# Performance work log

Measured on AMD Instinct MI355X. Metric: run time of the kernel, lower is better.

Reference implementation:

```python
import jax, jax.numpy as jnp
import numpy as np

B, S, K, N = 2, 512, 4096, 16384

def setup_inputs() -> dict:
    key = jax.random.key(0)
    k1, k2, k3, k4 = jax.random.split(key, 4)
    x = jax.random.normal(k1, (B, S, K), dtype=jnp.float32)
    # int8-valued quantized weight stored as int32 (values in [-128, 127])
    weight_quant = jax.random.randint(k2, (N, K), -128, 128, dtype=jnp.int32)
    # per-output-row scale, positive and away from zero (quantize_weight clamps min=1e-8)
    scale = jax.random.uniform(k3, (N,), dtype=jnp.float32, minval=0.001, maxval=0.02)
    bias = jax.random.normal(k4, (N,), dtype=jnp.float32)
    return {"x": x, "weight_quant": weight_quant, "scale": scale, "bias": bias}

def reference(x, weight_quant, scale, bias):
    # Dequantize: weight[n,k] = float(weight_quant[n,k]) * scale[n]
    weight = weight_quant.astype(jnp.float32) * scale[:, None]  # [N, K]
    # F.linear: x @ weight.T + bias
    return jnp.einsum('bsk,nk->bsn', x, weight) + bias
```

## Files before the change

### kernel.cpp

```cpp
#include <hip/hip_runtime.h>

typedef __attribute__((ext_vector_type(4))) float f32x4;
typedef __attribute__((ext_vector_type(4))) int   i32x4;

static constexpr int Kd = 4096, Nd = 16384, Md = 1024;
static constexpr int BK = 128;
static constexpr int NT = Kd / BK;


__device__ __forceinline__ void gload16(const char* g, char* l) {
    __builtin_amdgcn_global_load_lds(
        (const __attribute__((address_space(1))) void*)g,
        (__attribute__((address_space(3))) void*)l, 16, 0, 0);
}

__device__ __forceinline__ int pack4(int a, int b, int c, int d) {
    return (a & 255) | ((b & 255) << 8) | ((c & 255) << 16) | (d << 24);
}


__global__ __launch_bounds__(256) void convert_w_kernel(
    const int* __restrict__ wq, char* __restrict__ wb) {
    const int ngroups = (Nd / 16) * Kd;
    int g = blockIdx.x * 256 + threadIdx.x;
    const int stride = gridDim.x * 256;
    for (; g < ngroups; g += stride) {
        const int* src = wq + (size_t)g * 16;
        i32x4 a = *(const i32x4*)(src);
        i32x4 b = *(const i32x4*)(src + 4);
        i32x4 c = *(const i32x4*)(src + 8);
        i32x4 d = *(const i32x4*)(src + 12);
        i32x4 o;
        o[0] = pack4(a[0], a[1], a[2], a[3]);
        o[1] = pack4(b[0], b[1], b[2], b[3]);
        o[2] = pack4(c[0], c[1], c[2], c[3]);
        o[3] = pack4(d[0], d[1], d[2], d[3]);
        *(i32x4*)(wb + (size_t)g * 16) = o;
    }
}


__global__ __launch_bounds__(256) void convert_x_kernel(
    const float* __restrict__ x, char* __restrict__ xb, float* __restrict__ xs) {
    const int row = blockIdx.x;
    const int t   = threadIdx.x;
    const float* xr = x + (size_t)row * Kd;

    f32x4 v[4];
    float amax = 0.f;
    #pragma unroll
    for (int i = 0; i < 4; ++i) {
        v[i] = *(const f32x4*)(xr + t * 16 + i * 4);
        #pragma unroll
        for (int j = 0; j < 4; ++j) amax = fmaxf(amax, fabsf(v[i][j]));
    }
    #pragma unroll
    for (int off = 32; off; off >>= 1)
        amax = fmaxf(amax, __shfl_xor(amax, off));
    __shared__ float wmax[4];
    if ((t & 63) == 0) wmax[t >> 6] = amax;
    __syncthreads();
    amax = fmaxf(fmaxf(wmax[0], wmax[1]), fmaxf(wmax[2], wmax[3]));
    amax = fmaxf(amax, 1e-20f);

    const float inv = 127.0f / amax;
    i32x4 o;
    #pragma unroll
    for (int i = 0; i < 4; ++i) {
        int q[4];
        #pragma unroll
        for (int j = 0; j < 4; ++j) {
            int qi = __float2int_rn(v[i][j] * inv);
            qi = qi > 127 ? 127 : (qi < -127 ? -127 : qi);
            q[j] = qi;
        }
        o[i] = pack4(q[0], q[1], q[2], q[3]);
    }
    *(i32x4*)(xb + (size_t)row * Kd + t * 16) = o;
    if (t == 0) xs[row] = amax * (1.0f / 127.0f);
}


#define BARRIER() asm volatile("s_barrier" ::: "memory")

#define LGKM0_FENCE() do {                                                     \
    asm volatile("s_waitcnt lgkmcnt(0)");                                      \
    __builtin_amdgcn_sched_barrier(0);                                         \
} while (0)

#define STAGE_A(slot, h, kt) do {                                              \
    char* lb_ = &LDS[slot][0][h][w * 8][0];                                    \
    gload16(Ab + (aRow0 + (h) * 64) * (size_t)Kd + (kt) * BK + gcol, lb_);     \
    gload16(Ab + (aRow0 + (h) * 64 + 128) * (size_t)Kd + (kt) * BK + gcol,     \
            lb_ + 64 * 128);                                                   \
} while (0)

#define STAGE_B(slot, j, kt) do {                                              \
    char* lb_ = &LDS[slot][1][j][w * 8][0];                                    \
    gload16(Bw + (bRow0 + (j) * 32) * (size_t)Kd + (kt) * BK + gcol, lb_);     \
    gload16(Bw + (bRow0 + (j) * 32 + 128) * (size_t)Kd + (kt) * BK + gcol,     \
            lb_ + 64 * 128);                                                   \
} while (0)

#define READ_A(dst, slot, h) do {                                              \
    const char* lA_ = &LDS[slot][0][h][0][0];                                  \
    _Pragma("unroll")                                                          \
    for (int mi = 0; mi < 4; ++mi)                                             \
        _Pragma("unroll")                                                      \
        for (int kk = 0; kk < 2; ++kk) {                                       \
            const int row_ = wm * 64 + mi * 16 + lr;                           \
            const int col_ = (l4 * 16 + kk * 64) ^ xorv;                       \
            dst[mi][kk] = *(const i32x4*)(lA_ + row_ * 128 + col_);            \
        }                                                                      \
} while (0)

#define READ_B(dst, slot, j) do {                                              \
    const char* lB_ = &LDS[slot][1][j][0][0];                                  \
    _Pragma("unroll")                                                          \
    for (int ni = 0; ni < 2; ++ni)                                             \
        _Pragma("unroll")                                                      \
        for (int kk = 0; kk < 2; ++kk) {                                       \
            const int row_ = wn * 32 + ni * 16 + lr;                           \
            const int col_ = (l4 * 16 + kk * 64) ^ xorv;                       \
            dst[ni][kk] = *(const i32x4*)(lB_ + row_ * 128 + col_);            \
        }                                                                      \
} while (0)

#define MFMA_QUAD(h, j, AF, BF) do {                                           \
    __builtin_amdgcn_s_setprio(1);                                             \
    _Pragma("unroll")                                                          \
    for (int mi = 0; mi < 4; ++mi)                                             \
        _Pragma("unroll")                                                      \
        for (int ni = 0; ni < 2; ++ni)                                         \
            _Pragma("unroll")                                                  \
            for (int kk = 0; kk < 2; ++kk)                                     \
                acc[(h) * 4 + mi][(j) * 2 + ni] =                              \
                    __builtin_amdgcn_mfma_i32_16x16x64_i8(                     \
                        AF[mi][kk], BF[ni][kk],                                \
                        acc[(h) * 4 + mi][(j) * 2 + ni], 0, 0, 0);             \
    __builtin_amdgcn_s_setprio(0);                                             \
} while (0)

#define VMCNT_TILE(t)                                                          \
    do {                                                                       \
        if ((t) + 2 < NT) asm volatile("s_waitcnt vmcnt(4)" ::: "memory");     \
        else              asm volatile("s_waitcnt vmcnt(0)" ::: "memory");     \
    } while (0)

#define TILE(slot, oslot, t) do {                                              \
    i32x4 afA[4][2], afB[4][2], bfA[2][2], bfB[2][2];                          \
                                                       \
    READ_A(afA, slot, 0);                                                      \
    READ_B(bfA, slot, 0);                                                      \
    if ((t) + 1 < NT) STAGE_A(oslot, 1, (t) + 1);                              \
    BARRIER(); LGKM0_FENCE();                                                  \
    MFMA_QUAD(0, 0, afA, bfA);                                                 \
    BARRIER();                                                                 \
                                                       \
    READ_B(bfB, slot, 1);                                                      \
    if ((t) + 1 < NT) STAGE_B(oslot, 1, (t) + 1);                              \
    BARRIER(); LGKM0_FENCE();                                                  \
    MFMA_QUAD(0, 1, afA, bfB);                                                 \
    BARRIER();                                                                 \
                                                       \
    READ_A(afB, slot, 1);                                                      \
    if ((t) + 2 < NT) STAGE_A(slot, 0, (t) + 2);                               \
    BARRIER(); LGKM0_FENCE();                                                  \
    MFMA_QUAD(1, 0, afB, bfA);                                                 \
    BARRIER();                                                                 \
                          \
    if ((t) + 2 < NT) STAGE_B(slot, 0, (t) + 2);                               \
    VMCNT_TILE(t);                                                             \
    BARRIER();                                                                 \
    MFMA_QUAD(1, 1, afB, bfB);                                                 \
    BARRIER();                                                                 \
} while (0)

__global__ __launch_bounds__(512, 2) void gemm8_kernel(
    const char* __restrict__ Ab,
    const char* __restrict__ Bw,
    const float* __restrict__ sw,
    const float* __restrict__ xs,
    const float* __restrict__ bias,
    float* __restrict__ C) {

    __shared__ __align__(16) char LDS[2][2][2][128][128];

    const int tid = threadIdx.x;
    const int l   = tid & 63;
    const int w   = tid >> 6;
    const int wm  = w >> 2;
    const int wn  = w & 3;
    const int lr  = l & 15;
    const int l4  = l >> 4;
    const int xorv = (lr & 7) << 4;

    const int orig = blockIdx.x;
    const int work = (orig & 7) * 32 + (orig >> 3);
    const int gm0 = (work & 3) * 256;
    const int gn0 = (work >> 2) * 256;

    const int g_log = (l & 7) ^ ((l >> 3) & 7);
    const int gcol  = g_log * 16;
    const size_t aRow0 = (size_t)(gm0 + w * 8 + (l >> 3));
    const size_t bRow0 = (size_t)(gn0 + (w >> 2) * 64 + (w & 3) * 8 + (l >> 3));

    i32x4 acc[8][4];
    #pragma unroll
    for (int i = 0; i < 8; ++i)
        #pragma unroll
        for (int j = 0; j < 4; ++j) {
            i32x4 z = {0, 0, 0, 0};
            acc[i][j] = z;
        }

    STAGE_A(0, 0, 0); STAGE_B(0, 0, 0);
    STAGE_A(0, 1, 0); STAGE_B(0, 1, 0);
    STAGE_A(1, 0, 1); STAGE_B(1, 0, 1);
    asm volatile("s_waitcnt vmcnt(4)" ::: "memory");
    BARRIER();

    #pragma unroll 1
    for (int tt = 0; tt < NT / 2; ++tt) {
        TILE(0, 1, 2 * tt);
        TILE(1, 0, 2 * tt + 1);
    }

    #pragma unroll
    for (int bj = 0; bj < 4; ++bj) {
        const int gn = gn0 + wn * 64 + bj * 16 + lr;
        const float sc = sw[gn];
        const float bi = bias[gn];
        #pragma unroll
        for (int ai = 0; ai < 8; ++ai) {
            const int gm = gm0 + wm * 128 + ai * 16 + l4 * 4;
            #pragma unroll
            for (int r = 0; r < 4; ++r)
                C[(size_t)(gm + r) * Nd + gn] =
                    (float)acc[ai][bj][r] * (sc * xs[gm + r]) + bi;
        }
    }
}


__global__ __launch_bounds__(256) void naive_kernel(
    const float* __restrict__ x, const int* __restrict__ wq,
    const float* __restrict__ scale, const float* __restrict__ bias,
    float* __restrict__ out) {
    const int n = blockIdx.x * 256 + threadIdx.x;
    const int m = blockIdx.y;
    if (n >= Nd) return;
    const float* xr = x + (size_t)m * Kd;
    const int*   wr = wq + (size_t)n * Kd;
    float s = 0.f;
    for (int k = 0; k < Kd; ++k) s += xr[k] * (float)wr[k];
    out[(size_t)m * Nd + n] = s * scale[n] + bias[n];
}


extern "C" void kernel_launch(void* const* d_in, const int* in_sizes, int n_in,
                              void* d_out, int out_size, void* d_ws, size_t ws_size,
                              hipStream_t stream) {
    const float* x     = (const float*)d_in[0];
    const int*   wq    = (const int*)d_in[1];
    const float* scale = (const float*)d_in[2];
    const float* bias  = (const float*)d_in[3];
    float* out = (float*)d_out;

    const size_t w_bytes = (size_t)Nd * Kd;
    const size_t x_bytes = (size_t)Md * Kd;
    const size_t s_bytes = (size_t)Md * sizeof(float);
    if (ws_size >= w_bytes + x_bytes + s_bytes && d_ws != nullptr) {
        char*  wb = (char*)d_ws;
        char*  xb = wb + w_bytes;
        float* xs = (float*)(xb + x_bytes);
        convert_w_kernel<<<4096, 256, 0, stream>>>(wq, wb);
        convert_x_kernel<<<Md, 256, 0, stream>>>(x, xb, xs);
        gemm8_kernel<<<256, 512, 0, stream>>>(xb, wb, scale, xs, bias, out);
    } else {
        dim3 grid(Nd / 256, Md);
        naive_kernel<<<grid, 256, 0, stream>>>(x, wq, scale, bias, out);
    }
}
```

Measured before the change: 142.9 us.

## Pre-swizzle int8 weights into MFMA fragment order and load B directly to registers

The weight conversion kernel now writes int8 weights in a per-wave, per-lane MFMA fragment layout, so the GEMM can load B fragments straight from global memory into registers with coalesced 16-byte loads. This drops the B tiles from LDS, halving LDS use, and removes the B LDS reads along with several barriers. The main loop is rewritten with explicit vmcnt waits and double-buffered B fragment registers. The cost is more register pressure, and B is no longer shared through LDS, so each wave row re-reads its B fragments from global or cache.

```diff
diff --git a/kernel.cpp b/kernel.cpp
--- a/kernel.cpp
+++ b/kernel.cpp
@@ -21,21 +21,30 @@
 
 __global__ __launch_bounds__(256) void convert_w_kernel(
     const int* __restrict__ wq, char* __restrict__ wb) {
-    const int ngroups = (Nd / 16) * Kd;
-    int g = blockIdx.x * 256 + threadIdx.x;
+    const int total = (Nd / 256) * NT * 4 * 8 * 64;
+    int c = blockIdx.x * 256 + threadIdx.x;
     const int stride = gridDim.x * 256;
-    for (; g < ngroups; g += stride) {
-        const int* src = wq + (size_t)g * 16;
+    for (; c < total; c += stride) {
+        const int l   = c & 63;
+        const int fid = (c >> 6) & 7;
+        const int wn  = (c >> 9) & 3;
+        const int kt  = (c >> 11) & 31;
+        const int nt  = c >> 16;
+        const int j   = fid >> 2, ni = (fid >> 1) & 1, kkb = fid & 1;
+        const int lr  = l & 15,   l4 = l >> 4;
+        const int n   = nt * 256 + wn * 64 + j * 32 + ni * 16 + lr;
+        const int k0  = kt * 128 + kkb * 64 + l4 * 16;
+        const int* src = wq + (size_t)n * Kd + k0;
         i32x4 a = *(const i32x4*)(src);
         i32x4 b = *(const i32x4*)(src + 4);
-        i32x4 c = *(const i32x4*)(src + 8);
+        i32x4 cc = *(const i32x4*)(src + 8);
         i32x4 d = *(const i32x4*)(src + 12);
         i32x4 o;
         o[0] = pack4(a[0], a[1], a[2], a[3]);
         o[1] = pack4(b[0], b[1], b[2], b[3]);
-        o[2] = pack4(c[0], c[1], c[2], c[3]);
+        o[2] = pack4(cc[0], cc[1], cc[2], cc[3]);
         o[3] = pack4(d[0], d[1], d[2], d[3]);
-        *(i32x4*)(wb + (size_t)g * 16) = o;
+        *((i32x4*)wb + c) = o;
     }
 }
 
@@ -82,28 +91,40 @@
 
 
 #define BARRIER() asm volatile("s_barrier" ::: "memory")
+#define SBAR() __builtin_amdgcn_sched_barrier(0)
 
 #define LGKM0_FENCE() do {                                                     \
     asm volatile("s_waitcnt lgkmcnt(0)");                                      \
     __builtin_amdgcn_sched_barrier(0);                                         \
 } while (0)
 
-#define STAGE_A(slot, h, kt) do {                                              \
-    char* lb_ = &LDS[slot][0][h][w * 8][0];                                    \
-    gload16(Ab + (aRow0 + (h) * 64) * (size_t)Kd + (kt) * BK + gcol, lb_);     \
-    gload16(Ab + (aRow0 + (h) * 64 + 128) * (size_t)Kd + (kt) * BK + gcol,     \
-            lb_ + 64 * 128);                                                   \
-} while (0)
-
-#define STAGE_B(slot, j, kt) do {                                              \
-    char* lb_ = &LDS[slot][1][j][w * 8][0];                                    \
-    gload16(Bw + (bRow0 + (j) * 32) * (size_t)Kd + (kt) * BK + gcol, lb_);     \
-    gload16(Bw + (bRow0 + (j) * 32 + 128) * (size_t)Kd + (kt) * BK + gcol,     \
-            lb_ + 64 * 128);                                                   \
+#define VMCNT(n) do {                                                          \
+    asm volatile("s_waitcnt vmcnt(" #n ")" ::: "memory");                      \
+    __builtin_amdgcn_sched_barrier(0);                                         \
+} while (0)
+
+#define STAGE_AFULL(slot, kt) do {                                             \
+    _Pragma("unroll")                                                          \
+    for (int h_ = 0; h_ < 2; ++h_) {                                           \
+        char* lb_ = &LDSA[slot][h_][w * 8][0];                                 \
+        gload16(Ab + (aRow0 + h_ * 64) * (size_t)Kd + (kt) * BK + gcol, lb_);  \
+        gload16(Ab + (aRow0 + h_ * 64 + 128) * (size_t)Kd + (kt) * BK + gcol,  \
+                lb_ + 64 * 128);                                               \
+    }                                                                          \
+    __builtin_amdgcn_sched_barrier(0);                                         \
+} while (0)
+
+#define LOAD_BF(buf, kt, jj) do {                                              \
+    const i32x4* p_ = Bfr + (size_t)(kt) * 2048 + wn * 512 + (jj) * 256 + l;   \
+    buf[0][0] = p_[0];                                                         \
+    buf[0][1] = p_[64];                                                        \
+    buf[1][0] = p_[128];                                                       \
+    buf[1][1] = p_[192];                                                       \
+    __builtin_amdgcn_sched_barrier(0);                                         \
 } while (0)
 
 #define READ_A(dst, slot, h) do {                                              \
-    const char* lA_ = &LDS[slot][0][h][0][0];                                  \
+    const char* lA_ = &LDSA[slot][h][0][0];                                    \
     _Pragma("unroll")                                                          \
     for (int mi = 0; mi < 4; ++mi)                                             \
         _Pragma("unroll")                                                      \
@@ -111,18 +132,6 @@
             const int row_ = wm * 64 + mi * 16 + lr;                           \
             const int col_ = (l4 * 16 + kk * 64) ^ xorv;                       \
             dst[mi][kk] = *(const i32x4*)(lA_ + row_ * 128 + col_);            \
-        }                                                                      \
-} while (0)
-
-#define READ_B(dst, slot, j) do {                                              \
-    const char* lB_ = &LDS[slot][1][j][0][0];                                  \
-    _Pragma("unroll")                                                          \
-    for (int ni = 0; ni < 2; ++ni)                                             \
-        _Pragma("unroll")                                                      \
-        for (int kk = 0; kk < 2; ++kk) {                                       \
-            const int row_ = wn * 32 + ni * 16 + lr;                           \
-            const int col_ = (l4 * 16 + kk * 64) ^ xorv;                       \
-            dst[ni][kk] = *(const i32x4*)(lB_ + row_ * 128 + col_);            \
         }                                                                      \
 } while (0)
 
@@ -141,38 +150,25 @@
     __builtin_amdgcn_s_setprio(0);                                             \
 } while (0)
 
-#define VMCNT_TILE(t)                                                          \
-    do {                                                                       \
-        if ((t) + 2 < NT) asm volatile("s_waitcnt vmcnt(4)" ::: "memory");     \
-        else              asm volatile("s_waitcnt vmcnt(0)" ::: "memory");     \
-    } while (0)
-
-#define TILE(slot, oslot, t) do {                                              \
-    i32x4 afA[4][2], afB[4][2], bfA[2][2], bfB[2][2];                          \
-                                                       \
-    READ_A(afA, slot, 0);                                                      \
-    READ_B(bfA, slot, 0);                                                      \
-    if ((t) + 1 < NT) STAGE_A(oslot, 1, (t) + 1);                              \
-    BARRIER(); LGKM0_FENCE();                                                  \
-    MFMA_QUAD(0, 0, afA, bfA);                                                 \
-    BARRIER();                                                                 \
-                                                       \
-    READ_B(bfB, slot, 1);                                                      \
-    if ((t) + 1 < NT) STAGE_B(oslot, 1, (t) + 1);                              \
-    BARRIER(); LGKM0_FENCE();                                                  \
-    MFMA_QUAD(0, 1, afA, bfB);                                                 \
-    BARRIER();                                                                 \
-                                                       \
-    READ_A(afB, slot, 1);                                                      \
-    if ((t) + 2 < NT) STAGE_A(slot, 0, (t) + 2);                               \
-    BARRIER(); LGKM0_FENCE();                                                  \
-    MFMA_QUAD(1, 0, afB, bfA);                                                 \
-    BARRIER();                                                                 \
-                          \
-    if ((t) + 2 < NT) STAGE_B(slot, 0, (t) + 2);                               \
-    VMCNT_TILE(t);                                                             \
-    BARRIER();                                                                 \
-    MFMA_QUAD(1, 1, afB, bfB);                                                 \
+#define TILE(slot, oslot, BF0USE, BF0NXT, t) do {                              \
+    if ((t) + 1 < NT) {                                                        \
+        STAGE_AFULL(oslot, (t) + 1);                                           \
+        LOAD_BF(BF0NXT, (t) + 1, 0);                                           \
+    }                                                                          \
+    READ_A(af, slot, 0);                                                       \
+    if ((t) + 1 < NT) { VMCNT(12); } else { VMCNT(4); }                        \
+    LGKM0_FENCE();                                                             \
+    MFMA_QUAD(0, 0, af, BF0USE);                                               \
+    if ((t) + 1 < NT) { VMCNT(8); } else { VMCNT(0); }                         \
+    MFMA_QUAD(0, 1, af, bf1);                                                  \
+    READ_A(af, slot, 1);                                                       \
+    LGKM0_FENCE();                                                             \
+    MFMA_QUAD(1, 0, af, BF0USE);                                               \
+    MFMA_QUAD(1, 1, af, bf1);                                                  \
+    if ((t) + 1 < NT) {                                                        \
+        LOAD_BF(bf1, (t) + 1, 1);                                              \
+        VMCNT(4);                                                              \
+    }                                                                          \
     BARRIER();                                                                 \
 } while (0)
 
@@ -184,7 +180,7 @@
     const float* __restrict__ bias,
     float* __restrict__ C) {
 
-    __shared__ __align__(16) char LDS[2][2][2][128][128];
+    __shared__ __align__(16) char LDSA[2][2][128][128];
 
     const int tid = threadIdx.x;
     const int l   = tid & 63;
@@ -203,7 +199,12 @@
     const int g_log = (l & 7) ^ ((l >> 3) & 7);
     const int gcol  = g_log * 16;
     const size_t aRow0 = (size_t)(gm0 + w * 8 + (l >> 3));
-    const size_t bRow0 = (size_t)(gn0 + (w >> 2) * 64 + (w & 3) * 8 + (l >> 3));
+
+    const i32x4* Bfr = (const i32x4*)Bw + (size_t)(work >> 2) * 65536;
+
+    i32x4 af[4][2];
+    i32x4 bf0a[2][2], bf0b[2][2];
+    i32x4 bf1[2][2];
 
     i32x4 acc[8][4];
     #pragma unroll
@@ -214,16 +215,16 @@
             acc[i][j] = z;
         }
 
-    STAGE_A(0, 0, 0); STAGE_B(0, 0, 0);
-    STAGE_A(0, 1, 0); STAGE_B(0, 1, 0);
-    STAGE_A(1, 0, 1); STAGE_B(1, 0, 1);
-    asm volatile("s_waitcnt vmcnt(4)" ::: "memory");
+    STAGE_AFULL(0, 0);
+    LOAD_BF(bf0a, 0, 0);
+    LOAD_BF(bf1, 0, 1);
+    VMCNT(8);
     BARRIER();
 
     #pragma unroll 1
     for (int tt = 0; tt < NT / 2; ++tt) {
-        TILE(0, 1, 2 * tt);
-        TILE(1, 0, 2 * tt + 1);
+        TILE(0, 1, bf0a, bf0b, 2 * tt);
+        TILE(1, 0, bf0b, bf0a, 2 * tt + 1);
     }
 
     #pragma unroll
@@ -274,7 +275,7 @@
         char*  wb = (char*)d_ws;
         char*  xb = wb + w_bytes;
         float* xs = (float*)(xb + x_bytes);
-        convert_w_kernel<<<4096, 256, 0, stream>>>(wq, wb);
+        convert_w_kernel<<<8192, 256, 0, stream>>>(wq, wb);
         convert_x_kernel<<<Md, 256, 0, stream>>>(x, xb, xs);
         gemm8_kernel<<<256, 512, 0, stream>>>(xb, wb, scale, xs, bias, out);
     } else {
```

Measured after the change: 144.9 us. About the same (+1.4%).

## Stage GEMM tiles through registers and drop per-quad barriers

Applied to the files above, without the earlier changes.

Replaces the direct global-to-LDS loads (global_load_lds) with ordinary global loads into registers. Each next tile is loaded at the start of the current tile and written into the other LDS buffer, with its XOR swizzle, after the last MFMA quad. This removes the many barriers per tile, leaving one, and shortens prefetch depth from two staged half-tiles to a single full-tile double buffer. The cost is 32 more VGPRs under a 512-thread, 2-blocks-per-CU bound, plus explicit ds_writes and a vmcnt(0) wait before each tile switch.

```diff
diff --git a/kernel.cpp b/kernel.cpp
--- a/kernel.cpp
+++ b/kernel.cpp
@@ -7,12 +7,6 @@
 static constexpr int BK = 128;
 static constexpr int NT = Kd / BK;
 
-
-__device__ __forceinline__ void gload16(const char* g, char* l) {
-    __builtin_amdgcn_global_load_lds(
-        (const __attribute__((address_space(1))) void*)g,
-        (__attribute__((address_space(3))) void*)l, 16, 0, 0);
-}
 
 __device__ __forceinline__ int pack4(int a, int b, int c, int d) {
     return (a & 255) | ((b & 255) << 8) | ((c & 255) << 16) | (d << 24);
@@ -88,18 +82,33 @@
     __builtin_amdgcn_sched_barrier(0);                                         \
 } while (0)
 
-#define STAGE_A(slot, h, kt) do {                                              \
-    char* lb_ = &LDS[slot][0][h][w * 8][0];                                    \
-    gload16(Ab + (aRow0 + (h) * 64) * (size_t)Kd + (kt) * BK + gcol, lb_);     \
-    gload16(Ab + (aRow0 + (h) * 64 + 128) * (size_t)Kd + (kt) * BK + gcol,     \
-            lb_ + 64 * 128);                                                   \
-} while (0)
-
-#define STAGE_B(slot, j, kt) do {                                              \
-    char* lb_ = &LDS[slot][1][j][w * 8][0];                                    \
-    gload16(Bw + (bRow0 + (j) * 32) * (size_t)Kd + (kt) * BK + gcol, lb_);     \
-    gload16(Bw + (bRow0 + (j) * 32 + 128) * (size_t)Kd + (kt) * BK + gcol,     \
-            lb_ + 64 * 128);                                                   \
+#define VMCNT(n) do {                                                          \
+    asm volatile("s_waitcnt vmcnt(" #n ")" ::: "memory");                      \
+    __builtin_amdgcn_sched_barrier(0);                                         \
+} while (0)
+
+#define LOADG8(t) do {                                                         \
+    _Pragma("unroll")                                                          \
+    for (int i = 0; i < 4; ++i)                                                \
+        sA[i] = *(const i32x4*)(Ab +                                           \
+            (size_t)(gm0 + (i >> 1) * 64 + (i & 1) * 128 + qrow) * Kd          \
+            + (t) * BK + gc16);                                                \
+    _Pragma("unroll")                                                          \
+    for (int i = 0; i < 4; ++i)                                                \
+        sB[i] = *(const i32x4*)(Bw +                                           \
+            (size_t)(gn0 + (i >> 1) * 32 + (i & 1) * 128 + bQ) * Kd            \
+            + (t) * BK + gc16);                                                \
+    __builtin_amdgcn_sched_barrier(0);                                         \
+} while (0)
+
+#define WRITEL8(slot) do {                                                     \
+    _Pragma("unroll")                                                          \
+    for (int i = 0; i < 4; ++i)                                                \
+        *(i32x4*)(&LDS[slot][0][i >> 1][(i & 1) * 64 + qrow][swc]) = sA[i];    \
+    _Pragma("unroll")                                                          \
+    for (int i = 0; i < 4; ++i)                                                \
+        *(i32x4*)(&LDS[slot][1][i >> 1][(i & 1) * 64 + qrow][swc]) = sB[i];    \
+    __builtin_amdgcn_sched_barrier(0);                                         \
 } while (0)
 
 #define READ_A(dst, slot, h) do {                                              \
@@ -141,39 +150,26 @@
     __builtin_amdgcn_s_setprio(0);                                             \
 } while (0)
 
-#define VMCNT_TILE(t)                                                          \
-    do {                                                                       \
-        if ((t) + 2 < NT) asm volatile("s_waitcnt vmcnt(4)" ::: "memory");     \
-        else              asm volatile("s_waitcnt vmcnt(0)" ::: "memory");     \
-    } while (0)
-
 #define TILE(slot, oslot, t) do {                                              \
     i32x4 afA[4][2], afB[4][2], bfA[2][2], bfB[2][2];                          \
-                                                       \
+    if ((t) + 1 < NT) LOADG8((t) + 1);       \
     READ_A(afA, slot, 0);                                                      \
     READ_B(bfA, slot, 0);                                                      \
-    if ((t) + 1 < NT) STAGE_A(oslot, 1, (t) + 1);                              \
-    BARRIER(); LGKM0_FENCE();                                                  \
+    LGKM0_FENCE();                                                             \
     MFMA_QUAD(0, 0, afA, bfA);                                                 \
-    BARRIER();                                                                 \
-                                                       \
     READ_B(bfB, slot, 1);                                                      \
-    if ((t) + 1 < NT) STAGE_B(oslot, 1, (t) + 1);                              \
-    BARRIER(); LGKM0_FENCE();                                                  \
+    LGKM0_FENCE();                                                             \
     MFMA_QUAD(0, 1, afA, bfB);                                                 \
-    BARRIER();                                                                 \
-                                                       \
     READ_A(afB, slot, 1);                                                      \
-    if ((t) + 2 < NT) STAGE_A(slot, 0, (t) + 2);                               \
-    BARRIER(); LGKM0_FENCE();                                                  \
+    LGKM0_FENCE();                                                             \
     MFMA_QUAD(1, 0, afB, bfA);                                                 \
-    BARRIER();                                                                 \
-                          \
-    if ((t) + 2 < NT) STAGE_B(slot, 0, (t) + 2);                               \
-    VMCNT_TILE(t);                                                             \
-    BARRIER();                                                                 \
     MFMA_QUAD(1, 1, afB, bfB);                                                 \
-    BARRIER();                                                                 \
+    if ((t) + 1 < NT) {                                                        \
+        VMCNT(0);                                      \
+        WRITEL8(oslot);                  \
+        LGKM0_FENCE();                      \
+    }                                                                          \
+    BARRIER();                               \
 } while (0)
 
 __global__ __launch_bounds__(512, 2) void gemm8_kernel(
@@ -200,11 +196,14 @@
     const int gm0 = (work & 3) * 256;
     const int gn0 = (work >> 2) * 256;
 
-    const int g_log = (l & 7) ^ ((l >> 3) & 7);
-    const int gcol  = g_log * 16;
-    const size_t aRow0 = (size_t)(gm0 + w * 8 + (l >> 3));
-    const size_t bRow0 = (size_t)(gn0 + (w >> 2) * 64 + (w & 3) * 8 + (l >> 3));
-
+    const int qrow = w * 8 + (l >> 3);
+    const int bQ   = (w >> 2) * 64 + (w & 3) * 8 + (l >> 3);
+    const int gc16 = (l & 7) * 16;
+    const int swc  = gc16 ^ ((l >> 3) << 4);
+
+    i32x4 sA[4], sB[4];
+
+    f32x4 accf; (void)accf;
     i32x4 acc[8][4];
     #pragma unroll
     for (int i = 0; i < 8; ++i)
@@ -214,10 +213,10 @@
             acc[i][j] = z;
         }
 
-    STAGE_A(0, 0, 0); STAGE_B(0, 0, 0);
-    STAGE_A(0, 1, 0); STAGE_B(0, 1, 0);
-    STAGE_A(1, 0, 1); STAGE_B(1, 0, 1);
-    asm volatile("s_waitcnt vmcnt(4)" ::: "memory");
+    LOADG8(0);
+    VMCNT(0);
+    WRITEL8(0);
+    LGKM0_FENCE();
     BARRIER();
 
     #pragma unroll 1
```

Result: slower. 172.7 us (+20.8%).
